# Performance work log

Measured on AMD Instinct MI355X. Metric: run time of the kernel, lower is better.

## Reference

```python
import jax, jax.numpy as jnp
import numpy as np

B, L, S, D, C, H = 8, 64, 2048, 1024, 1024, 16
HD = D // H
EPS = 1e-5


def _lin(x, w, b):
    # torch Linear: w is [out, in]
    return jnp.einsum('...i,oi->...o', x, w) + b


def _ln(x, g, b):
    m = jnp.mean(x, axis=-1, keepdims=True)
    v = jnp.var(x, axis=-1, keepdims=True)
    return (x - m) * jax.lax.rsqrt(v + EPS) * g + b


def setup_inputs() -> dict:
    key = jax.random.key(0)
    ks = jax.random.split(key, 24)

    def w(k, shape, scale=0.02):
        return jax.random.normal(k, shape, dtype=jnp.float32) * scale

    return {
        'latents': jax.random.normal(ks[0], (B, L, D), dtype=jnp.float32),
        'context': jax.random.normal(ks[1], (B, S, C), dtype=jnp.float32),
        'context_mask': jax.random.randint(ks[2], (B, S), 0, 2),
        'q_w': w(ks[3], (D, D)), 'q_b': jnp.zeros((D,), jnp.float32),
        'k_w': w(ks[4], (D, C)), 'k_b': jnp.zeros((D,), jnp.float32),
        'v_w': w(ks[5], (D, C)), 'v_b': jnp.zeros((D,), jnp.float32),
        # nn.MultiheadAttention internal in_proj (split into q/k/v parts) + out_proj
        'in_wq': w(ks[6], (D, D)), 'in_bq': jnp.zeros((D,), jnp.float32),
        'in_wk': w(ks[7], (D, D)), 'in_bk': jnp.zeros((D,), jnp.float32),
        'in_wv': w(ks[8], (D, D)), 'in_bv': jnp.zeros((D,), jnp.float32),
        'out_w': w(ks[9], (D, D)), 'out_b': jnp.zeros((D,), jnp.float32),
        'ln1_g': jnp.ones((D,), jnp.float32), 'ln1_b': jnp.zeros((D,), jnp.float32),
        'ln2_g': jnp.ones((D,), jnp.float32), 'ln2_b': jnp.zeros((D,), jnp.float32),
        'ff_w1': w(ks[10], (4 * D, D)), 'ff_b1': jnp.zeros((4 * D,), jnp.float32),
        'ff_w2': w(ks[11], (D, 4 * D)), 'ff_b2': jnp.zeros((D,), jnp.float32),
    }


def reference(latents, context, context_mask,
              q_w, q_b, k_w, k_b, v_w, v_b,
              in_wq, in_bq, in_wk, in_bk, in_wv, in_bv,
              out_w, out_b, ln1_g, ln1_b, ln2_g, ln2_b,
              ff_w1, ff_b1, ff_w2, ff_b2):
    # external projections
    q = _lin(latents, q_w, q_b)        # [B,L,D]
    k = _lin(context, k_w, k_b)        # [B,S,D]
    v = _lin(context, v_w, v_b)        # [B,S,D]
    # MultiheadAttention internal in_proj
    qh = _lin(q, in_wq, in_bq).reshape(B, L, H, HD)
    kh = _lin(k, in_wk, in_bk).reshape(B, S, H, HD)
    vh = _lin(v, in_wv, in_bv).reshape(B, S, H, HD)
    scores = jnp.einsum('blhd,bshd->bhls', qh, kh) / np.sqrt(HD)  # [B,H,L,S]
    pad = (context_mask == 0)[:, None, None, :]                    # key_padding_mask
    scores = jnp.where(pad, -jnp.inf, scores)
    w = jax.nn.softmax(scores, axis=-1)                            # [B,H,L,S]
    attn = jnp.einsum('bhls,bshd->blhd', w, vh).reshape(B, L, D)
    attn_out = _lin(attn, out_w, out_b)
    attn_weights = jnp.mean(w, axis=1)                             # averaged over heads [B,L,S]
    x = _ln(latents + attn_out, ln1_g, ln1_b)
    ff = _lin(jax.nn.gelu(_lin(x, ff_w1, ff_b1), approximate=False), ff_w2, ff_b2)
    out = _ln(x + ff, ln2_g, ln2_b)
    return (out, attn_weights)
```

## Files before the change

### kernel.cpp

```cpp
#include <hip/hip_runtime.h>
#include <hip/hip_bf16.h>

typedef unsigned short u16;
typedef unsigned int u32;
typedef __attribute__((ext_vector_type(8))) short bf16x8;
typedef __attribute__((ext_vector_type(4))) float f32x4;

typedef __attribute__((address_space(1))) const u32 as1_u32;
typedef __attribute__((address_space(3))) u32 as3_u32;

#define MFMA16(a, b, c) __builtin_amdgcn_mfma_f32_16x16x32_bf16(a, b, c, 0, 0, 0)

__device__ __forceinline__ void gld16(const void* g, void* l) {
  __builtin_amdgcn_global_load_lds((as1_u32*)g, (as3_u32*)l, 16, 0, 0);
}

__device__ __forceinline__ float b2f(u16 u) { return __uint_as_float(((u32)u) << 16); }
__device__ __forceinline__ u16 f2b(float f) {
  u32 x = __float_as_uint(f);
  u32 r = (x + 0x7fffu + ((x >> 16) & 1u)) >> 16;
  return (u16)r;
}

__device__ __forceinline__ float wave_red(float v) {
  for (int o = 32; o; o >>= 1) v += __shfl_down(v, o);
  return v;
}

__global__ __launch_bounds__(256) void fused_cast_kernel(
    const float* __restrict__ s0, const float* __restrict__ s1,
    const float* __restrict__ s2, const float* __restrict__ s3,
    const float* __restrict__ s4, const float* __restrict__ s5,
    const float* __restrict__ s6, const float* __restrict__ s7,
    u16* __restrict__ d0, u16* __restrict__ d1, u16* __restrict__ d2,
    u16* __restrict__ d3, u16* __restrict__ d4, u16* __restrict__ d5,
    u16* __restrict__ d6, u16* __restrict__ d7) {
  const unsigned base = blockIdx.x * 1024u;
  const float* src;
  u16* dst;
  unsigned off;
  if (base < 16777216u)      { src = s0; dst = d0; off = 0u; }
  else if (base < 17301504u) { src = s1; dst = d1; off = 16777216u; }
  else if (base < 18350080u) { src = s2; dst = d2; off = 17301504u; }
  else if (base < 19398656u) { src = s3; dst = d3; off = 18350080u; }
  else if (base < 20447232u) { src = s4; dst = d4; off = 19398656u; }
  else if (base < 21495808u) { src = s5; dst = d5; off = 20447232u; }
  else if (base < 25690112u) { src = s6; dst = d6; off = 21495808u; }
  else                       { src = s7; dst = d7; off = 25690112u; }
  const unsigned i = base - off + threadIdx.x * 4u;
  float4 v = *reinterpret_cast<const float4*>(src + i);
  ushort4 o;
  o.x = f2b(v.x); o.y = f2b(v.y); o.z = f2b(v.z); o.w = f2b(v.w);
  *reinterpret_cast<ushort4*>(dst + i) = o;
}

__global__ __launch_bounds__(256) void castT_kernel(const float* __restrict__ in,
                                                    u16* __restrict__ out) {
  __shared__ u16 sm[32][33];
  const int r0 = blockIdx.y * 32, c0 = blockIdx.x * 32;
  const int t = threadIdx.x;
  const int r = t >> 3, c4 = (t & 7) * 4;
  float4 v = *reinterpret_cast<const float4*>(in + (size_t)(r0 + r) * 1024 + c0 + c4);
  sm[c4 + 0][r] = f2b(v.x);
  sm[c4 + 1][r] = f2b(v.y);
  sm[c4 + 2][r] = f2b(v.z);
  sm[c4 + 3][r] = f2b(v.w);
  __syncthreads();
  ushort4 o;
  o.x = sm[r][c4 + 0]; o.y = sm[r][c4 + 1]; o.z = sm[r][c4 + 2]; o.w = sm[r][c4 + 3];
  *reinterpret_cast<ushort4*>(out + (size_t)(c0 + r) * 1024 + r0 + c4) = o;
}

__global__ __launch_bounds__(256) void biascomp_kernel(const float* __restrict__ A,
                                                       const float* __restrict__ b,
                                                       const float* __restrict__ b2,
                                                       float* __restrict__ out) {
  __shared__ float red[4];
  const int row = blockIdx.x;
  const int t = threadIdx.x;
  float4 va = *reinterpret_cast<const float4*>(A + (size_t)row * 1024 + t * 4);
  float4 vb = *reinterpret_cast<const float4*>(b + t * 4);
  float s = va.x * vb.x + va.y * vb.y + va.z * vb.z + va.w * vb.w;
  s = wave_red(s);
  if ((t & 63) == 0) red[t >> 6] = s;
  __syncthreads();
  if (t == 0) out[row] = red[0] + red[1] + red[2] + red[3] + b2[row];
}

template <int EPI, int BIASM, int SWZ>
__global__ __launch_bounds__(256) void gemm_bt(
    const u16* __restrict__ A, const u16* __restrict__ W, const float* __restrict__ bias,
    void* __restrict__ Cout, int M, int N, int K, int lda, int ldw, int ldc,
    long long bsA, long long bsW, long long bsC) {
  __shared__ u16 a_sm[128 * 32];
  __shared__ u16 b_sm[128 * 32];
  int bx = blockIdx.x, by = blockIdx.y, bz = blockIdx.z;
  if (SWZ) {
    const int gx = gridDim.x, gy = gridDim.y;
    const int lin = bx + gx * (by + gy * bz);
    const int nwg = gx * gy * gridDim.z;
    const int swz = (lin & 7) * (nwg >> 3) + (lin >> 3);
    bx = swz % gx;
    const int t2 = swz / gx;
    by = t2 % gy;
    bz = t2 / gy;
  }
  const int t = threadIdx.x;
  const int lane = t & 63;
  const int wv = t >> 6;
  const int wm = wv >> 1, wn = wv & 1;
  const int l15 = lane & 15, l4 = lane >> 4;
  const long long zb = bz;

  const u16* Ab = A + zb * bsA;
  const u16* Wb = W + zb * bsW;

  const u16* ag = Ab + (size_t)(by * 128 + (t >> 2)) * lda + (t & 3) * 8;
  const u16* wg = Wb + (size_t)(bx * 128 + (t >> 2)) * ldw + (t & 3) * 8;
  u16* ad = a_sm + t * 8;
  u16* bd = b_sm + t * 8;

  f32x4 acc[4][4] = {};

  for (int k0 = 0; k0 < K; k0 += 32) {
    gld16(ag, ad);
    gld16(ag + (size_t)64 * lda, ad + 64 * 32);
    gld16(wg, bd);
    gld16(wg + (size_t)64 * ldw, bd + 64 * 32);
    ag += 32; wg += 32;
    __syncthreads();
    bf16x8 af[4], bf[4];
#pragma unroll
    for (int m = 0; m < 4; m++)
      af[m] = *reinterpret_cast<const bf16x8*>(&a_sm[(wm * 64 + m * 16 + l15) * 32 + l4 * 8]);
#pragma unroll
    for (int n = 0; n < 4; n++)
      bf[n] = *reinterpret_cast<const bf16x8*>(&b_sm[(wn * 64 + n * 16 + l15) * 32 + l4 * 8]);
#pragma unroll
    for (int m = 0; m < 4; m++)
#pragma unroll
      for (int n = 0; n < 4; n++)
        acc[m][n] = MFMA16(af[m], bf[n], acc[m][n]);
    __syncthreads();
  }

  const int gm0 = by * 128 + wm * 64;
  const int gn0 = bx * 128 + wn * 64;
  float* cf = reinterpret_cast<float*>(Cout) + zb * bsC;
  u16* cb = reinterpret_cast<u16*>(Cout) + zb * bsC;
#pragma unroll
  for (int m = 0; m < 4; m++) {
#pragma unroll
    for (int n = 0; n < 4; n++) {
      const int col = gn0 + n * 16 + l15;
      float bc = (BIASM == 1) ? bias[col] : 0.f;
#pragma unroll
      for (int r = 0; r < 4; r++) {
        const int row = gm0 + m * 16 + l4 * 4 + r;
        float v = acc[m][n][r];
        if (BIASM == 1) v += bc;
        if (BIASM == 2) v += bias[row];
        if (EPI == 2) v = 0.5f * v * (1.0f + erff(v * 0.70710678118654752f));
        if (EPI == 0) cf[(size_t)row * ldc + col] = v;
        else          cb[(size_t)row * ldc + col] = f2b(v);
      }
    }
  }
}

template <int EPI, int BIASM>
__global__ __launch_bounds__(256) void gemm64(
    const u16* __restrict__ A, const u16* __restrict__ W, const float* __restrict__ bias,
    void* __restrict__ Cout, int M, int N, int K, int lda, int ldw, int ldc) {
  __shared__ u16 a_sm[64 * 32];
  __shared__ u16 b_sm[64 * 32];
  const int t = threadIdx.x;
  const int lane = t & 63;
  const int wv = t >> 6;
  const int wm = wv >> 1, wn = wv & 1;
  const int l15 = lane & 15, l4 = lane >> 4;

  const u16* ag = A + (size_t)(blockIdx.y * 64 + (t >> 2)) * lda + (t & 3) * 8;
  const u16* wg = W + (size_t)(blockIdx.x * 64 + (t >> 2)) * ldw + (t & 3) * 8;
  u16* ad = a_sm + t * 8;
  u16* bd = b_sm + t * 8;

  f32x4 acc[2][2] = {};

  for (int k0 = 0; k0 < K; k0 += 32) {
    gld16(ag, ad);
    gld16(wg, bd);
    ag += 32; wg += 32;
    __syncthreads();
    bf16x8 af[2], bf[2];
#pragma unroll
    for (int m = 0; m < 2; m++)
      af[m] = *reinterpret_cast<const bf16x8*>(&a_sm[(wm * 32 + m * 16 + l15) * 32 + l4 * 8]);
#pragma unroll
    for (int n = 0; n < 2; n++)
      bf[n] = *reinterpret_cast<const bf16x8*>(&b_sm[(wn * 32 + n * 16 + l15) * 32 + l4 * 8]);
#pragma unroll
    for (int m = 0; m < 2; m++)
#pragma unroll
      for (int n = 0; n < 2; n++)
        acc[m][n] = MFMA16(af[m], bf[n], acc[m][n]);
    __syncthreads();
  }

  const int gm0 = blockIdx.y * 64 + wm * 32;
  const int gn0 = blockIdx.x * 64 + wn * 32;
  float* cf = reinterpret_cast<float*>(Cout);
  u16* cb = reinterpret_cast<u16*>(Cout);
#pragma unroll
  for (int m = 0; m < 2; m++) {
#pragma unroll
    for (int n = 0; n < 2; n++) {
      const int col = gn0 + n * 16 + l15;
      float bc = (BIASM == 1) ? bias[col] : 0.f;
#pragma unroll
      for (int r = 0; r < 4; r++) {
        const int row = gm0 + m * 16 + l4 * 4 + r;
        float v = acc[m][n][r];
        if (BIASM == 1) v += bc;
        if (BIASM == 2) v += bias[row];
        if (EPI == 2) v = 0.5f * v * (1.0f + erff(v * 0.70710678118654752f));
        if (EPI == 0) cf[(size_t)row * ldc + col] = v;
        else          cb[(size_t)row * ldc + col] = f2b(v);
      }
    }
  }
}

__global__ __launch_bounds__(256) void gemm64sk(
    const u16* __restrict__ A, const u16* __restrict__ W, float* __restrict__ part,
    int N, int Kc, int lda, int ldw) {
  __shared__ u16 a_sm[64 * 32];
  __shared__ u16 b_sm[64 * 32];
  const int t = threadIdx.x;
  const int lane = t & 63;
  const int wv = t >> 6;
  const int wm = wv >> 1, wn = wv & 1;
  const int l15 = lane & 15, l4 = lane >> 4;
  const int z = blockIdx.z;

  const u16* ag = A + (size_t)(blockIdx.y * 64 + (t >> 2)) * lda + z * Kc + (t & 3) * 8;
  const u16* wg = W + (size_t)(blockIdx.x * 64 + (t >> 2)) * ldw + z * Kc + (t & 3) * 8;
  u16* ad = a_sm + t * 8;
  u16* bd = b_sm + t * 8;

  f32x4 acc[2][2] = {};

  for (int k0 = 0; k0 < Kc; k0 += 32) {
    gld16(ag, ad);
    gld16(wg, bd);
    ag += 32; wg += 32;
    __syncthreads();
    bf16x8 af[2], bf[2];
#pragma unroll
    for (int m = 0; m < 2; m++)
      af[m] = *reinterpret_cast<const bf16x8*>(&a_sm[(wm * 32 + m * 16 + l15) * 32 + l4 * 8]);
#pragma unroll
    for (int n = 0; n < 2; n++)
      bf[n] = *reinterpret_cast<const bf16x8*>(&b_sm[(wn * 32 + n * 16 + l15) * 32 + l4 * 8]);
#pragma unroll
    for (int m = 0; m < 2; m++)
#pragma unroll
      for (int n = 0; n < 2; n++)
        acc[m][n] = MFMA16(af[m], bf[n], acc[m][n]);
    __syncthreads();
  }

  const int Mtot = gridDim.y * 64;
  float* po = part + (size_t)z * Mtot * N;
  const int gm0 = blockIdx.y * 64 + wm * 32;
  const int gn0 = blockIdx.x * 64 + wn * 32;
#pragma unroll
  for (int m = 0; m < 2; m++) {
#pragma unroll
    for (int n = 0; n < 2; n++) {
      const int col = gn0 + n * 16 + l15;
#pragma unroll
      for (int r = 0; r < 4; r++) {
        const int row = gm0 + m * 16 + l4 * 4 + r;
        po[(size_t)row * N + col] = acc[m][n][r];
      }
    }
  }
}

__global__ __launch_bounds__(256) void redb_kernel(const float* __restrict__ p,
                                                   const float* __restrict__ bias,
                                                   u16* __restrict__ out) {
  const int i = (blockIdx.x * 256 + threadIdx.x) * 4;
  const int col = i & 1023;
  float4 v0 = *reinterpret_cast<const float4*>(p + i);
  float4 v1 = *reinterpret_cast<const float4*>(p + 524288 + i);
  float4 vb = *reinterpret_cast<const float4*>(bias + col);
  ushort4 o;
  o.x = f2b(v0.x + v1.x + vb.x);
  o.y = f2b(v0.y + v1.y + vb.y);
  o.z = f2b(v0.z + v1.z + vb.z);
  o.w = f2b(v0.w + v1.w + vb.w);
  *reinterpret_cast<ushort4*>(out + i) = o;
}

__global__ __launch_bounds__(256) void scores_kernel(const u16* __restrict__ QH,
                                                     const u16* __restrict__ KH,
                                                     const int* __restrict__ mask,
                                                     u16* __restrict__ probs) {
  __shared__ u16 q_sm[64 * 64];
  __shared__ u16 k_sm[256 * 64];
  int bx = blockIdx.x, by = blockIdx.y;
  {
    const int lin = bx + 8 * by;
    const int swz = (lin & 7) * 128 + (lin >> 3);
    bx = swz & 7;
    by = swz >> 3;
  }
  const int bh = by;
  const int b = bh >> 4, h = bh & 15;
  const int sc = bx;
  const int t = threadIdx.x;
  const int lane = t & 63;
  const int wv = t >> 6;
  const int l15 = lane & 15, l4 = lane >> 4;
  const int x7 = l15 & 7;

  const int r = t >> 3;
  const int cs = (t & 7) ^ (r & 7);
  {
    const u16* src = QH + (size_t)(b * 64 + r) * 1024 + h * 64 + cs * 8;
    u16* dst = q_sm + t * 8;
    gld16(src, dst);
    gld16(src + (size_t)32 * 1024, dst + 32 * 64);
  }
  {
    const u16* src = KH + (size_t)(b * 2048 + sc * 256 + r) * 1024 + h * 64 + cs * 8;
    u16* dst = k_sm + t * 8;
#pragma unroll
    for (int i = 0; i < 8; i++)
      gld16(src + (size_t)i * 32 * 1024, dst + i * 32 * 64);
  }
  __syncthreads();

  f32x4 acc[4][4] = {};
#pragma unroll
  for (int ks = 0; ks < 2; ks++) {
    bf16x8 af[4], bf[4];
#pragma unroll
    for (int m = 0; m < 4; m++)
      af[m] = *reinterpret_cast<const bf16x8*>(
          &q_sm[(m * 16 + l15) * 64 + ((ks * 4 + l4) ^ x7) * 8]);
#pragma unroll
    for (int n = 0; n < 4; n++)
      bf[n] = *reinterpret_cast<const bf16x8*>(
          &k_sm[(wv * 64 + n * 16 + l15) * 64 + ((ks * 4 + l4) ^ x7) * 8]);
#pragma unroll
    for (int m = 0; m < 4; m++)
#pragma unroll
      for (int n = 0; n < 4; n++)
        acc[m][n] = MFMA16(af[m], bf[n], acc[m][n]);
  }

#pragma unroll
  for (int n = 0; n < 4; n++) {
    const int sg = sc * 256 + wv * 64 + n * 16 + l15;
    const bool keep = mask[b * 2048 + sg] != 0;
#pragma unroll
    for (int m = 0; m < 4; m++) {
#pragma unroll
      for (int r2 = 0; r2 < 4; r2++) {
        const int row = m * 16 + l4 * 4 + r2;
        float p = keep ? __expf(acc[m][n][r2] * 0.125f) : 0.f;
        probs[((size_t)bh * 64 + row) * 2048 + sg] = f2b(p);
      }
    }
  }
}

__global__ __launch_bounds__(256) void rowsum_kernel(const u16* __restrict__ probs,
                                                     float* __restrict__ inv) {
  __shared__ float red[4];
  const int row = blockIdx.x;
  const int t = threadIdx.x;
  uint4 r4 = *reinterpret_cast<const uint4*>(probs + (size_t)row * 2048 + t * 8);
  float s = b2f((u16)(r4.x & 0xffffu)) + b2f((u16)(r4.x >> 16)) +
            b2f((u16)(r4.y & 0xffffu)) + b2f((u16)(r4.y >> 16)) +
            b2f((u16)(r4.z & 0xffffu)) + b2f((u16)(r4.z >> 16)) +
            b2f((u16)(r4.w & 0xffffu)) + b2f((u16)(r4.w >> 16));
  s = wave_red(s);
  if ((t & 63) == 0) red[t >> 6] = s;
  __syncthreads();
  if (t == 0) inv[row] = 1.0f / (red[0] + red[1] + red[2] + red[3]);
}

__global__ __launch_bounds__(256) void pv_part_kernel(const u16* __restrict__ probs,
                                                      const u16* __restrict__ VT,
                                                      float* __restrict__ part) {
  __shared__ u16 a_sm[64 * 64];
  __shared__ u16 b_sm[64 * 64];
  int bx = blockIdx.x, by = blockIdx.y;
  {
    const int lin = bx + 4 * by;
    const int swz = (lin & 7) * 64 + (lin >> 3);
    bx = swz & 3;
    by = swz >> 2;
  }
  const int c = bx;
  const int bh = by;
  const int b = bh >> 4, h = bh & 15;
  const u16* Ab = probs + (size_t)bh * 64 * 2048;
  const u16* Bb = VT + ((size_t)b * 1024 + h * 64) * 2048;
  const int t = threadIdx.x;
  const int lane = t & 63;
  const int wv = t >> 6;
  const int wm = wv >> 1, wn = wv & 1;
  const int l15 = lane & 15, l4 = lane >> 4;
  const int x7 = l15 & 7;

  const int r = t >> 3;
  const int cs = (t & 7) ^ (r & 7);

  f32x4 acc[2][2] = {};
  for (int k0 = c * 512; k0 < c * 512 + 512; k0 += 64) {
    const u16* as = Ab + (size_t)r * 2048 + k0 + cs * 8;
    const u16* bs = Bb + (size_t)r * 2048 + k0 + cs * 8;
    u16* ad = a_sm + t * 8;
    u16* bd = b_sm + t * 8;
    gld16(as, ad);
    gld16(as + (size_t)32 * 2048, ad + 32 * 64);
    gld16(bs, bd);
    gld16(bs + (size_t)32 * 2048, bd + 32 * 64);
    __syncthreads();
#pragma unroll
    for (int ks = 0; ks < 2; ks++) {
      bf16x8 af[2], bf[2];
#pragma unroll
      for (int m = 0; m < 2; m++)
        af[m] = *reinterpret_cast<const bf16x8*>(
            &a_sm[(wm * 32 + m * 16 + l15) * 64 + ((ks * 4 + l4) ^ x7) * 8]);
#pragma unroll
      for (int n = 0; n < 2; n++)
        bf[n] = *reinterpret_cast<const bf16x8*>(
            &b_sm[(wn * 32 + n * 16 + l15) * 64 + ((ks * 4 + l4) ^ x7) * 8]);
#pragma unroll
      for (int m = 0; m < 2; m++)
#pragma unroll
        for (int n = 0; n < 2; n++)
          acc[m][n] = MFMA16(af[m], bf[n], acc[m][n]);
    }
    __syncthreads();
  }

  float* po = part + ((size_t)(bh * 4 + c)) * 4096;
#pragma unroll
  for (int m = 0; m < 2; m++) {
#pragma unroll
    for (int n = 0; n < 2; n++) {
#pragma unroll
      for (int r2 = 0; r2 < 4; r2++) {
        const int l = wm * 32 + m * 16 + l4 * 4 + r2;
        const int hd = wn * 32 + n * 16 + l15;
        po[l * 64 + hd] = acc[m][n][r2];
      }
    }
  }
}

__global__ __launch_bounds__(256) void pv_reduce_kernel(const float* __restrict__ part,
                                                        const float* __restrict__ inv,
                                                        u16* __restrict__ attn) {
  const int t = threadIdx.x;
  const int e0 = (blockIdx.x * 256 + t) * 4;
  const int bh = e0 >> 12;
  const int r = e0 & 4095;
  const int l = r >> 6, hd = r & 63;
  const int b = bh >> 4, h = bh & 15;
  const float* p = part + ((size_t)bh * 4) * 4096 + r;
  float4 v0 = *reinterpret_cast<const float4*>(p);
  float4 v1 = *reinterpret_cast<const float4*>(p + 4096);
  float4 v2 = *reinterpret_cast<const float4*>(p + 8192);
  float4 v3 = *reinterpret_cast<const float4*>(p + 12288);
  const float sc = inv[bh * 64 + l];
  ushort4 o;
  o.x = f2b((v0.x + v1.x + v2.x + v3.x) * sc);
  o.y = f2b((v0.y + v1.y + v2.y + v3.y) * sc);
  o.z = f2b((v0.z + v1.z + v2.z + v3.z) * sc);
  o.w = f2b((v0.w + v1.w + v2.w + v3.w) * sc);
  *reinterpret_cast<ushort4*>(attn + (size_t)(b * 64 + l) * 1024 + h * 64 + hd) = o;
}

__global__ __launch_bounds__(256) void mean_kernel(const u16* __restrict__ probs,
                                                   const float* __restrict__ inv,
                                                   float* __restrict__ outw) {
  __shared__ float s_inv[16];
  const int bl = blockIdx.x;
  const int b = bl >> 6, l = bl & 63;
  const int t = threadIdx.x;
  if (t < 16) s_inv[t] = inv[(b * 16 + t) * 64 + l] * 0.0625f;
  __syncthreads();
  float av[8] = {0.f, 0.f, 0.f, 0.f, 0.f, 0.f, 0.f, 0.f};
  for (int h = 0; h < 16; h++) {
    uint4 r4 = *reinterpret_cast<const uint4*>(
        probs + ((size_t)((b * 16 + h) * 64 + l)) * 2048 + t * 8);
    float sc = s_inv[h];
    av[0] += b2f((u16)(r4.x & 0xffffu)) * sc; av[1] += b2f((u16)(r4.x >> 16)) * sc;
    av[2] += b2f((u16)(r4.y & 0xffffu)) * sc; av[3] += b2f((u16)(r4.y >> 16)) * sc;
    av[4] += b2f((u16)(r4.z & 0xffffu)) * sc; av[5] += b2f((u16)(r4.z >> 16)) * sc;
    av[6] += b2f((u16)(r4.w & 0xffffu)) * sc; av[7] += b2f((u16)(r4.w >> 16)) * sc;
  }
  float* o = outw + (size_t)bl * 2048 + t * 8;
  *reinterpret_cast<float4*>(o) = make_float4(av[0], av[1], av[2], av[3]);
  *reinterpret_cast<float4*>(o + 4) = make_float4(av[4], av[5], av[6], av[7]);
}

template <int NP>
__global__ __launch_bounds__(256) void lnp_kernel(const float* __restrict__ a,
                                                  const float* __restrict__ parts,
                                                  const float* __restrict__ bias,
                                                  const float* __restrict__ g,
                                                  const float* __restrict__ bet,
                                                  float* __restrict__ outf,
                                                  u16* __restrict__ outb) {
  __shared__ float red[8];
  __shared__ float mv[2];
  const int row = blockIdx.x;
  const int t = threadIdx.x;
  const size_t idx = (size_t)row * 1024 + t * 4;
  const float4 va = *reinterpret_cast<const float4*>(a + idx);
  const float4 vb = *reinterpret_cast<const float4*>(bias + t * 4);
  float x0 = va.x + vb.x, x1 = va.y + vb.y, x2 = va.z + vb.z, x3 = va.w + vb.w;
#pragma unroll
  for (int p = 0; p < NP; p++) {
    const float4 vp = *reinterpret_cast<const float4*>(parts + (size_t)p * 524288 + idx);
    x0 += vp.x; x1 += vp.y; x2 += vp.z; x3 += vp.w;
  }
  float s = x0 + x1 + x2 + x3;
  float q = x0 * x0 + x1 * x1 + x2 * x2 + x3 * x3;
  s = wave_red(s);
  q = wave_red(q);
  if ((t & 63) == 0) { red[t >> 6] = s; red[4 + (t >> 6)] = q; }
  __syncthreads();
  if (t == 0) {
    float S = red[0] + red[1] + red[2] + red[3];
    float Q = red[4] + red[5] + red[6] + red[7];
    float mu = S * (1.f / 1024.f);
    float var = Q * (1.f / 1024.f) - mu * mu;
    mv[0] = mu;
    mv[1] = rsqrtf(var + 1e-5f);
  }
  __syncthreads();
  const float mu = mv[0], rs = mv[1];
  const float4 vg = *reinterpret_cast<const float4*>(g + t * 4);
  const float4 ve = *reinterpret_cast<const float4*>(bet + t * 4);
  float y0 = (x0 - mu) * rs * vg.x + ve.x;
  float y1 = (x1 - mu) * rs * vg.y + ve.y;
  float y2 = (x2 - mu) * rs * vg.z + ve.z;
  float y3 = (x3 - mu) * rs * vg.w + ve.w;
  *reinterpret_cast<float4*>(outf + idx) = make_float4(y0, y1, y2, y3);
  if (outb) {
    ushort4 o;
    o.x = f2b(y0); o.y = f2b(y1); o.z = f2b(y2); o.w = f2b(y3);
    *reinterpret_cast<ushort4*>(outb + idx) = o;
  }
}

extern "C" void kernel_launch(void* const* d_in, const int* in_sizes, int n_in,
                              void* d_out, int out_size, void* d_ws, size_t ws_size,
                              hipStream_t stream) {
  const float* latents = (const float*)d_in[0];
  const float* context = (const float*)d_in[1];
  const int* cmask = (const int*)d_in[2];
  const float* q_w = (const float*)d_in[3];   const float* q_b = (const float*)d_in[4];
  const float* k_w = (const float*)d_in[5];   const float* k_b = (const float*)d_in[6];
  const float* v_w = (const float*)d_in[7];   const float* v_b = (const float*)d_in[8];
  const float* in_wq = (const float*)d_in[9]; const float* in_bq = (const float*)d_in[10];
  const float* in_wk = (const float*)d_in[11]; const float* in_bk = (const float*)d_in[12];
  const float* in_wv = (const float*)d_in[13]; const float* in_bv = (const float*)d_in[14];
  const float* out_w = (const float*)d_in[15]; const float* out_b = (const float*)d_in[16];
  const float* ln1_g = (const float*)d_in[17]; const float* ln1_b = (const float*)d_in[18];
  const float* ln2_g = (const float*)d_in[19]; const float* ln2_b = (const float*)d_in[20];
  const float* ff_w1 = (const float*)d_in[21]; const float* ff_b1 = (const float*)d_in[22];
  const float* ff_w2 = (const float*)d_in[23]; const float* ff_b2 = (const float*)d_in[24];

  char* wsb = (char*)d_ws;
  size_t off = 0;
  auto alloc = [&](size_t bytes) -> char* {
    char* p = wsb + off;
    off = (off + bytes + 255) & ~(size_t)255;
    return p;
  };

  u16* ctx_b = (u16*)alloc(33554432);
  u16* kh    = (u16*)alloc(33554432);
  u16* vt    = (u16*)alloc(33554432);
  u16* probs = (u16*)alloc(33554432);
  float* pvp = (float*)alloc(8388608);
  u16* lat_b = (u16*)alloc(1048576);
  u16* wiq   = (u16*)alloc(2097152);
  u16* wik   = (u16*)alloc(2097152);
  u16* wiv   = (u16*)alloc(2097152);
  u16* qwT   = (u16*)alloc(2097152);
  u16* kwT   = (u16*)alloc(2097152);
  u16* vwT   = (u16*)alloc(2097152);
  u16* wqc   = (u16*)alloc(2097152);
  u16* wkc   = (u16*)alloc(2097152);
  u16* wvc   = (u16*)alloc(2097152);
  u16* wob   = (u16*)alloc(2097152);
  u16* wf1b  = (u16*)alloc(8388608);
  u16* wf2b  = (u16*)alloc(8388608);
  float* b_qc = (float*)alloc(4096);
  float* b_kc = (float*)alloc(4096);
  float* b_vc = (float*)alloc(4096);
  float* inv_rs = (float*)alloc(32768);
  float* partsQ = (float*)alloc(4194304);
  float* partsO = (float*)alloc(4194304);
  float* partsF = (float*)alloc(16777216);

  char* ar = (char*)ctx_b;
  u16* qhb    = (u16*)(ar);
  u16* attn_b = (u16*)(ar + 1048576);
  u16* xb     = (u16*)(ar + 2097152);
  u16* h1     = (u16*)(ar + 3145728);
  float* xf   = (float*)(ar + 7340032);

  fused_cast_kernel<<<dim3(29184), 256, 0, stream>>>(
      context, latents, in_wq, in_wk, in_wv, out_w, ff_w1, ff_w2,
      ctx_b, lat_b, wiq, wik, wiv, wob, wf1b, wf2b);

  castT_kernel<<<dim3(32, 32), 256, 0, stream>>>(q_w, qwT);
  castT_kernel<<<dim3(32, 32), 256, 0, stream>>>(k_w, kwT);
  castT_kernel<<<dim3(32, 32), 256, 0, stream>>>(v_w, vwT);

  biascomp_kernel<<<dim3(1024), 256, 0, stream>>>(in_wq, q_b, in_bq, b_qc);
  biascomp_kernel<<<dim3(1024), 256, 0, stream>>>(in_wk, k_b, in_bk, b_kc);
  biascomp_kernel<<<dim3(1024), 256, 0, stream>>>(in_wv, v_b, in_bv, b_vc);

  gemm_bt<1, 0, 1><<<dim3(8, 8, 3), 256, 0, stream>>>(wiq, qwT, nullptr, wqc,
      1024, 1024, 1024, 1024, 1024, 1024, 1048576, 1048576, 1048576);

  gemm_bt<1, 1, 1><<<dim3(8, 128, 1), 256, 0, stream>>>(ctx_b, wkc, b_kc, kh,
      16384, 1024, 1024, 1024, 1024, 1024, 0, 0, 0);
  gemm_bt<1, 2, 1><<<dim3(16, 8, 8), 256, 0, stream>>>(wvc, ctx_b, b_vc, vt,
      1024, 2048, 1024, 1024, 1024, 2048, 0, 2048LL * 1024, 1024LL * 2048);

  gemm64sk<<<dim3(16, 8, 2), 256, 0, stream>>>(lat_b, wqc, partsQ, 1024, 512, 1024, 1024);
  redb_kernel<<<dim3(512), 256, 0, stream>>>(partsQ, b_qc, qhb);

  scores_kernel<<<dim3(8, 128), 256, 0, stream>>>(qhb, kh, cmask, probs);
  rowsum_kernel<<<dim3(8192), 256, 0, stream>>>(probs, inv_rs);
  pv_part_kernel<<<dim3(4, 128), 256, 0, stream>>>(probs, vt, pvp);
  pv_reduce_kernel<<<dim3(512), 256, 0, stream>>>(pvp, inv_rs, attn_b);
  mean_kernel<<<dim3(512), 256, 0, stream>>>(probs, inv_rs, (float*)d_out + 524288);

  gemm64sk<<<dim3(16, 8, 2), 256, 0, stream>>>(attn_b, wob, partsO, 1024, 512, 1024, 1024);
  lnp_kernel<2><<<dim3(512), 256, 0, stream>>>(latents, partsO, out_b, ln1_g, ln1_b, xf, xb);

  gemm64<2, 1><<<dim3(64, 8), 256, 0, stream>>>(xb, wf1b, ff_b1, h1,
      512, 4096, 1024, 1024, 1024, 4096);
  gemm64sk<<<dim3(16, 8, 4), 256, 0, stream>>>(h1, wf2b, partsF, 1024, 1024, 4096, 4096);
  lnp_kernel<4><<<dim3(512), 256, 0, stream>>>(xf, partsF, ff_b2, ln2_g, ln2_b,
                                               (float*)d_out, nullptr);
}
```

Before: 450.7 us.

## Add 256x256 double-buffered GEMM for K/V projections, fuse rowsum into scores

Replaces the 128-tile GEMMs for the large context K and V projections with a new 512-thread, 256x256-tile kernel. It double-buffers 64-wide K slices in LDS through async global-to-LDS loads and uses setprio around the MFMA groups. The softmax row sums are now accumulated inside the scores kernel with shuffles and atomics, which removes the separate rowsum pass over the probs buffer. The three castT and three biascomp launches are merged into single launches. The trade-offs are atomic accumulation order (non-deterministic sums), high register and LDS pressure in the big-tile kernel, and the zeroing of the sums buffer inside the cast kernel.

```diff
diff --git a/kernel.cpp b/kernel.cpp
--- a/kernel.cpp
+++ b/kernel.cpp
@@ -34,7 +34,11 @@
     const float* __restrict__ s6, const float* __restrict__ s7,
     u16* __restrict__ d0, u16* __restrict__ d1, u16* __restrict__ d2,
     u16* __restrict__ d3, u16* __restrict__ d4, u16* __restrict__ d5,
-    u16* __restrict__ d6, u16* __restrict__ d7) {
+    u16* __restrict__ d6, u16* __restrict__ d7, float* __restrict__ sums) {
+  if (blockIdx.x == 0) {
+#pragma unroll
+    for (int i = 0; i < 32; i++) sums[threadIdx.x + i * 256] = 0.f;
+  }
   const unsigned base = blockIdx.x * 1024u;
   const float* src;
   u16* dst;
@@ -54,9 +58,13 @@
   *reinterpret_cast<ushort4*>(dst + i) = o;
 }
 
-__global__ __launch_bounds__(256) void castT_kernel(const float* __restrict__ in,
-                                                    u16* __restrict__ out) {
+__global__ __launch_bounds__(256) void castT3_kernel(const float* __restrict__ s0,
+                                                     const float* __restrict__ s1,
+                                                     const float* __restrict__ s2,
+                                                     u16* __restrict__ out) {
   __shared__ u16 sm[32][33];
+  const float* in = blockIdx.z == 0 ? s0 : (blockIdx.z == 1 ? s1 : s2);
+  u16* o = out + (size_t)blockIdx.z * 1048576;
   const int r0 = blockIdx.y * 32, c0 = blockIdx.x * 32;
   const int t = threadIdx.x;
   const int r = t >> 3, c4 = (t & 7) * 4;
@@ -66,17 +74,22 @@
   sm[c4 + 2][r] = f2b(v.z);
   sm[c4 + 3][r] = f2b(v.w);
   __syncthreads();
-  ushort4 o;
-  o.x = sm[r][c4 + 0]; o.y = sm[r][c4 + 1]; o.z = sm[r][c4 + 2]; o.w = sm[r][c4 + 3];
-  *reinterpret_cast<ushort4*>(out + (size_t)(c0 + r) * 1024 + r0 + c4) = o;
-}
-
-__global__ __launch_bounds__(256) void biascomp_kernel(const float* __restrict__ A,
-                                                       const float* __restrict__ b,
-                                                       const float* __restrict__ b2,
-                                                       float* __restrict__ out) {
+  ushort4 q;
+  q.x = sm[r][c4 + 0]; q.y = sm[r][c4 + 1]; q.z = sm[r][c4 + 2]; q.w = sm[r][c4 + 3];
+  *reinterpret_cast<ushort4*>(o + (size_t)(c0 + r) * 1024 + r0 + c4) = q;
+}
+
+__global__ __launch_bounds__(256) void biascomp3_kernel(
+    const float* __restrict__ A0, const float* __restrict__ A1, const float* __restrict__ A2,
+    const float* __restrict__ b0, const float* __restrict__ b1, const float* __restrict__ b2,
+    const float* __restrict__ c0, const float* __restrict__ c1, const float* __restrict__ c2,
+    float* __restrict__ out) {
   __shared__ float red[4];
-  const int row = blockIdx.x;
+  const int sel = blockIdx.x >> 10;
+  const int row = blockIdx.x & 1023;
+  const float* A = sel == 0 ? A0 : (sel == 1 ? A1 : A2);
+  const float* b = sel == 0 ? b0 : (sel == 1 ? b1 : b2);
+  const float* c = sel == 0 ? c0 : (sel == 1 ? c1 : c2);
   const int t = threadIdx.x;
   float4 va = *reinterpret_cast<const float4*>(A + (size_t)row * 1024 + t * 4);
   float4 vb = *reinterpret_cast<const float4*>(b + t * 4);
@@ -84,7 +97,7 @@
   s = wave_red(s);
   if ((t & 63) == 0) red[t >> 6] = s;
   __syncthreads();
-  if (t == 0) out[row] = red[0] + red[1] + red[2] + red[3] + b2[row];
+  if (t == 0) out[sel * 1024 + row] = red[0] + red[1] + red[2] + red[3] + c[row];
 }
 
 template <int EPI, int BIASM, int SWZ>
@@ -168,6 +181,131 @@
   }
 }
 
+template <int BIASM>
+__global__ __launch_bounds__(512, 2) void gemm8p(
+    const u16* __restrict__ A, const u16* __restrict__ W, const float* __restrict__ bias,
+    u16* __restrict__ Cout, int K, int lda, int ldw, int ldc,
+    long long bsA, long long bsW, long long bsC) {
+  __shared__ u16 lds[2][2][256 * 64];
+  int bx = blockIdx.x, by = blockIdx.y, bz = blockIdx.z;
+  {
+    const int gx = gridDim.x, gy = gridDim.y;
+    const int lin = bx + gx * (by + gy * bz);
+    const int nwg = gx * gy * gridDim.z;
+    const int swz = (lin & 7) * (nwg >> 3) + (lin >> 3);
+    bx = swz % gx;
+    const int t2 = swz / gx;
+    by = t2 % gy;
+    bz = t2 / gy;
+  }
+  const int t = threadIdx.x;
+  const int lane = t & 63;
+  const int w = t >> 6;
+  const int wm = w >> 2;
+  const int wn = w & 3;
+  const int l15 = lane & 15, l4 = lane >> 4;
+  const long long zb = bz;
+  const u16* Ab = A + zb * bsA;
+  const u16* Wb = W + zb * bsW;
+
+  const int lr = lane >> 3;
+  const int lc = lane & 7;
+  const int scs = lc ^ lr;
+  const int arow_base = wm * 128 + wn * 32;
+  const int brow_base = (wn >> 1) * 128 + (wm * 2 + (wn & 1)) * 32;
+
+  const u16* ag = Ab + (size_t)(by * 256 + arow_base + lr) * lda + scs * 8;
+  const u16* wg = Wb + (size_t)(bx * 256 + brow_base + lr) * ldw + scs * 8;
+
+  f32x4 acc[8][4] = {};
+  const int NT = K >> 6;
+
+#pragma unroll
+  for (int j = 0; j < 4; j++) {
+    gld16(ag + (size_t)(j * 8) * lda, &lds[0][0][(arow_base + j * 8) * 64] + lane * 8);
+    gld16(wg + (size_t)(j * 8) * ldw, &lds[0][1][(brow_base + j * 8) * 64] + lane * 8);
+  }
+  asm volatile("s_waitcnt vmcnt(0)" ::: "memory");
+  __builtin_amdgcn_s_barrier();
+
+  for (int kt = 0; kt < NT; kt++) {
+    const int cur = kt & 1;
+    if (kt + 1 < NT) {
+      const int k0n = (kt + 1) << 6;
+#pragma unroll
+      for (int j = 0; j < 4; j++) {
+        gld16(ag + (size_t)(j * 8) * lda + k0n,
+              &lds[cur ^ 1][0][(arow_base + j * 8) * 64] + lane * 8);
+        gld16(wg + (size_t)(j * 8) * ldw + k0n,
+              &lds[cur ^ 1][1][(brow_base + j * 8) * 64] + lane * 8);
+      }
+    }
+    const u16* As = &lds[cur][0][0];
+    const u16* Bs = &lds[cur][1][0];
+    bf16x8 afr[8], bfr[4];
+#pragma unroll
+    for (int kh = 0; kh < 2; kh++) {
+#pragma unroll
+      for (int mi = 0; mi < 8; mi++) {
+        const int ra = wm * 128 + mi * 16 + l15;
+        afr[mi] = *reinterpret_cast<const bf16x8*>(
+            &As[ra * 64 + (((kh * 4 + l4) ^ (ra & 7)) * 8)]);
+      }
+#pragma unroll
+      for (int ni = 0; ni < 2; ni++) {
+        const int rb = wn * 64 + ni * 16 + l15;
+        bfr[ni] = *reinterpret_cast<const bf16x8*>(
+            &Bs[rb * 64 + (((kh * 4 + l4) ^ (rb & 7)) * 8)]);
+      }
+      __builtin_amdgcn_s_setprio(1);
+#pragma unroll
+      for (int mi = 0; mi < 8; mi++) {
+        acc[mi][0] = MFMA16(afr[mi], bfr[0], acc[mi][0]);
+        acc[mi][1] = MFMA16(afr[mi], bfr[1], acc[mi][1]);
+      }
+      __builtin_amdgcn_s_setprio(0);
+      __builtin_amdgcn_s_barrier();
+#pragma unroll
+      for (int ni = 0; ni < 2; ni++) {
+        const int rb = wn * 64 + (ni + 2) * 16 + l15;
+        bfr[2 + ni] = *reinterpret_cast<const bf16x8*>(
+            &Bs[rb * 64 + (((kh * 4 + l4) ^ (rb & 7)) * 8)]);
+      }
+      __builtin_amdgcn_s_setprio(1);
+#pragma unroll
+      for (int mi = 0; mi < 8; mi++) {
+        acc[mi][2] = MFMA16(afr[mi], bfr[2], acc[mi][2]);
+        acc[mi][3] = MFMA16(afr[mi], bfr[3], acc[mi][3]);
+      }
+      __builtin_amdgcn_s_setprio(0);
+      __builtin_amdgcn_s_barrier();
+    }
+    if (kt + 1 < NT) {
+      asm volatile("s_waitcnt vmcnt(0)" ::: "memory");
+      __builtin_amdgcn_sched_barrier(0);
+    }
+    __builtin_amdgcn_s_barrier();
+  }
+
+  const int gm0 = by * 256 + wm * 128;
+  const int gn0 = bx * 256 + wn * 64;
+  u16* cb = Cout + zb * bsC;
+#pragma unroll
+  for (int mi = 0; mi < 8; mi++) {
+#pragma unroll
+    for (int ni = 0; ni < 4; ni++) {
+      const int col = gn0 + ni * 16 + l15;
+      float bc = (BIASM == 1) ? bias[col] : 0.f;
+#pragma unroll
+      for (int r = 0; r < 4; r++) {
+        const int row = gm0 + mi * 16 + l4 * 4 + r;
+        float v = acc[mi][ni][r] + ((BIASM == 1) ? bc : bias[row]);
+        cb[(size_t)row * ldc + col] = f2b(v);
+      }
+    }
+  }
+}
+
 template <int EPI, int BIASM>
 __global__ __launch_bounds__(256) void gemm64(
     const u16* __restrict__ A, const u16* __restrict__ W, const float* __restrict__ bias,
@@ -307,9 +445,11 @@
 __global__ __launch_bounds__(256) void scores_kernel(const u16* __restrict__ QH,
                                                      const u16* __restrict__ KH,
                                                      const int* __restrict__ mask,
-                                                     u16* __restrict__ probs) {
+                                                     u16* __restrict__ probs,
+                                                     float* __restrict__ sums) {
   __shared__ u16 q_sm[64 * 64];
   __shared__ u16 k_sm[256 * 64];
+  __shared__ float srs[64];
   int bx = blockIdx.x, by = blockIdx.y;
   {
     const int lin = bx + 8 * by;
@@ -341,6 +481,7 @@
     for (int i = 0; i < 8; i++)
       gld16(src + (size_t)i * 32 * 1024, dst + i * 32 * 64);
   }
+  if (t < 64) srs[t] = 0.f;
   __syncthreads();
 
   f32x4 acc[4][4] = {};
@@ -362,6 +503,7 @@
         acc[m][n] = MFMA16(af[m], bf[n], acc[m][n]);
   }
 
+  float rs[4][4] = {};
 #pragma unroll
   for (int n = 0; n < 4; n++) {
     const int sg = sc * 256 + wv * 64 + n * 16 + l15;
@@ -373,25 +515,30 @@
         const int row = m * 16 + l4 * 4 + r2;
         float p = keep ? __expf(acc[m][n][r2] * 0.125f) : 0.f;
         probs[((size_t)bh * 64 + row) * 2048 + sg] = f2b(p);
-      }
-    }
-  }
-}
-
-__global__ __launch_bounds__(256) void rowsum_kernel(const u16* __restrict__ probs,
-                                                     float* __restrict__ inv) {
-  __shared__ float red[4];
-  const int row = blockIdx.x;
-  const int t = threadIdx.x;
-  uint4 r4 = *reinterpret_cast<const uint4*>(probs + (size_t)row * 2048 + t * 8);
-  float s = b2f((u16)(r4.x & 0xffffu)) + b2f((u16)(r4.x >> 16)) +
-            b2f((u16)(r4.y & 0xffffu)) + b2f((u16)(r4.y >> 16)) +
-            b2f((u16)(r4.z & 0xffffu)) + b2f((u16)(r4.z >> 16)) +
-            b2f((u16)(r4.w & 0xffffu)) + b2f((u16)(r4.w >> 16));
-  s = wave_red(s);
-  if ((t & 63) == 0) red[t >> 6] = s;
+        rs[m][r2] += p;
+      }
+    }
+  }
+#pragma unroll
+  for (int m = 0; m < 4; m++)
+#pragma unroll
+    for (int r2 = 0; r2 < 4; r2++) {
+      float v = rs[m][r2];
+      v += __shfl_xor(v, 1);
+      v += __shfl_xor(v, 2);
+      v += __shfl_xor(v, 4);
+      v += __shfl_xor(v, 8);
+      rs[m][r2] = v;
+    }
+  if (l15 == 0) {
+#pragma unroll
+    for (int m = 0; m < 4; m++)
+#pragma unroll
+      for (int r2 = 0; r2 < 4; r2++)
+        atomicAdd(&srs[m * 16 + l4 * 4 + r2], rs[m][r2]);
+  }
   __syncthreads();
-  if (t == 0) inv[row] = 1.0f / (red[0] + red[1] + red[2] + red[3]);
+  if (t < 64) atomicAdd(&sums[bh * 64 + t], srs[t]);
 }
 
 __global__ __launch_bounds__(256) void pv_part_kernel(const u16* __restrict__ probs,
@@ -468,7 +615,7 @@
 }
 
 __global__ __launch_bounds__(256) void pv_reduce_kernel(const float* __restrict__ part,
-                                                        const float* __restrict__ inv,
+                                                        const float* __restrict__ sums,
                                                         u16* __restrict__ attn) {
   const int t = threadIdx.x;
   const int e0 = (blockIdx.x * 256 + t) * 4;
@@ -481,7 +628,7 @@
   float4 v1 = *reinterpret_cast<const float4*>(p + 4096);
   float4 v2 = *reinterpret_cast<const float4*>(p + 8192);
   float4 v3 = *reinterpret_cast<const float4*>(p + 12288);
-  const float sc = inv[bh * 64 + l];
+  const float sc = 1.0f / sums[bh * 64 + l];
   ushort4 o;
   o.x = f2b((v0.x + v1.x + v2.x + v3.x) * sc);
   o.y = f2b((v0.y + v1.y + v2.y + v3.y) * sc);
@@ -491,13 +638,13 @@
 }
 
 __global__ __launch_bounds__(256) void mean_kernel(const u16* __restrict__ probs,
-                                                   const float* __restrict__ inv,
+                                                   const float* __restrict__ sums,
                                                    float* __restrict__ outw) {
   __shared__ float s_inv[16];
   const int bl = blockIdx.x;
   const int b = bl >> 6, l = bl & 63;
   const int t = threadIdx.x;
-  if (t < 16) s_inv[t] = inv[(b * 16 + t) * 64 + l] * 0.0625f;
+  if (t < 16) s_inv[t] = 0.0625f / sums[(b * 16 + t) * 64 + l];
   __syncthreads();
   float av[8] = {0.f, 0.f, 0.f, 0.f, 0.f, 0.f, 0.f, 0.f};
   for (int h = 0; h < 16; h++) {
@@ -612,7 +759,7 @@
   float* b_qc = (float*)alloc(4096);
   float* b_kc = (float*)alloc(4096);
   float* b_vc = (float*)alloc(4096);
-  float* inv_rs = (float*)alloc(32768);
+  float* sums = (float*)alloc(32768);
   float* partsQ = (float*)alloc(4194304);
   float* partsO = (float*)alloc(4194304);
   float* partsF = (float*)alloc(16777216);
@@ -626,32 +773,29 @@
 
   fused_cast_kernel<<<dim3(29184), 256, 0, stream>>>(
       context, latents, in_wq, in_wk, in_wv, out_w, ff_w1, ff_w2,
-      ctx_b, lat_b, wiq, wik, wiv, wob, wf1b, wf2b);
-
-  castT_kernel<<<dim3(32, 32), 256, 0, stream>>>(q_w, qwT);
-  castT_kernel<<<dim3(32, 32), 256, 0, stream>>>(k_w, kwT);
-  castT_kernel<<<dim3(32, 32), 256, 0, stream>>>(v_w, vwT);
-
-  biascomp_kernel<<<dim3(1024), 256, 0, stream>>>(in_wq, q_b, in_bq, b_qc);
-  biascomp_kernel<<<dim3(1024), 256, 0, stream>>>(in_wk, k_b, in_bk, b_kc);
-  biascomp_kernel<<<dim3(1024), 256, 0, stream>>>(in_wv, v_b, in_bv, b_vc);
+      ctx_b, lat_b, wiq, wik, wiv, wob, wf1b, wf2b, sums);
+
+  castT3_kernel<<<dim3(32, 32, 3), 256, 0, stream>>>(q_w, k_w, v_w, qwT);
+
+  biascomp3_kernel<<<dim3(3072), 256, 0, stream>>>(in_wq, in_wk, in_wv,
+                                                   q_b, k_b, v_b,
+                                                   in_bq, in_bk, in_bv, b_qc);
 
   gemm_bt<1, 0, 1><<<dim3(8, 8, 3), 256, 0, stream>>>(wiq, qwT, nullptr, wqc,
       1024, 1024, 1024, 1024, 1024, 1024, 1048576, 1048576, 1048576);
 
-  gemm_bt<1, 1, 1><<<dim3(8, 128, 1), 256, 0, stream>>>(ctx_b, wkc, b_kc, kh,
-      16384, 1024, 1024, 1024, 1024, 1024, 0, 0, 0);
-  gemm_bt<1, 2, 1><<<dim3(16, 8, 8), 256, 0, stream>>>(wvc, ctx_b, b_vc, vt,
-      1024, 2048, 1024, 1024, 1024, 2048, 0, 2048LL * 1024, 1024LL * 2048);
+  gemm8p<1><<<dim3(4, 64, 1), 512, 0, stream>>>(ctx_b, wkc, b_kc, kh,
+      1024, 1024, 1024, 1024, 0, 0, 0);
+  gemm8p<2><<<dim3(8, 4, 8), 512, 0, stream>>>(wvc, ctx_b, b_vc, vt,
+      1024, 1024, 1024, 2048, 0, 2048LL * 1024, 1024LL * 2048);
 
   gemm64sk<<<dim3(16, 8, 2), 256, 0, stream>>>(lat_b, wqc, partsQ, 1024, 512, 1024, 1024);
   redb_kernel<<<dim3(512), 256, 0, stream>>>(partsQ, b_qc, qhb);
 
-  scores_kernel<<<dim3(8, 128), 256, 0, stream>>>(qhb, kh, cmask, probs);
-  rowsum_kernel<<<dim3(8192), 256, 0, stream>>>(probs, inv_rs);
+  scores_kernel<<<dim3(8, 128), 256, 0, stream>>>(qhb, kh, cmask, probs, sums);
   pv_part_kernel<<<dim3(4, 128), 256, 0, stream>>>(probs, vt, pvp);
-  pv_reduce_kernel<<<dim3(512), 256, 0, stream>>>(pvp, inv_rs, attn_b);
-  mean_kernel<<<dim3(512), 256, 0, stream>>>(probs, inv_rs, (float*)d_out + 524288);
+  pv_reduce_kernel<<<dim3(512), 256, 0, stream>>>(pvp, sums, attn_b);
+  mean_kernel<<<dim3(512), 256, 0, stream>>>(probs, sums, (float*)d_out + 524288);
 
   gemm64sk<<<dim3(16, 8, 2), 256, 0, stream>>>(attn_b, wob, partsO, 1024, 512, 1024, 1024);
   lnp_kernel<2><<<dim3(512), 256, 0, stream>>>(latents, partsO, out_b, ln1_g, ln1_b, xf, xb);
```

Measured after the change: 401.2 us. 11.0% less time.
